# Kernel optimization log

Measured on AMD Instinct MI355X. Metric: run time of the kernel, lower is better.

Reference implementation:

```python
import jax, jax.numpy as jnp
import numpy as np

N = 100000
E = 2000000
F = 64          # in_features == out_features (required by attention * h_j)
BETA = 0.5
NEG_SLOPE = 0.01  # torch F.leaky_relu default


def setup_inputs() -> dict:
    key = jax.random.key(0)
    k1, k2, k3, k4, k5, k6 = jax.random.split(key, 6)
    h = jax.random.normal(k1, (N, F), dtype=jnp.float32)
    adj = jax.random.randint(k2, (2, E), 0, N, dtype=jnp.int64)
    amount = jax.random.uniform(k3, (E,), dtype=jnp.float32)
    count = jax.random.uniform(k4, (E,), dtype=jnp.float32)
    fc_w = jax.random.normal(k5, (F, 2 * F), dtype=jnp.float32) * (1.0 / np.sqrt(2 * F))
    fc_b = jax.random.normal(k6, (F,), dtype=jnp.float32) * 0.01
    return {"h": h, "adj": adj, "amount": amount, "count": count,
            "fc_w": fc_w, "fc_b": fc_b}


def _minmax_norm(x):
    lo, hi = x.min(), x.max()
    return (x - lo) / (hi - lo + 1e-8)


def reference(h, adj, amount, count, fc_w, fc_b):
    # per-edge weight from normalized amount/count
    edge_weight = BETA * _minmax_norm(amount) + (1.0 - BETA) * _minmax_norm(count)  # [E]

    src, dst = adj[0], adj[1]
    h_i = h[src]                     # [E, F]
    h_j = h[dst]                     # [E, F]
    h_cat = jnp.concatenate([h_i, h_j], axis=1)  # [E, 2F]

    score = jnp.einsum('ef,of->eo', h_cat, fc_w) + fc_b  # [E, F_out]
    score = jnp.where(score >= 0, score, NEG_SLOPE * score)  # leaky_relu
    score = score * edge_weight[:, None]

    # softmax over ALL edges (dim 0), per feature, as in the original
    attention = jax.nn.softmax(score, axis=0)  # [E, F]

    agg = jnp.zeros_like(h).at[src].add(attention * h_j)  # scatter-add -> [N, F]
    return agg
```

## Files before the change

kernel.cpp:

```cpp
#include <hip/hip_runtime.h>
#include <hip/hip_fp16.h>
#include <math.h>

#define FDIM   64
#define NB     16
#define BSHIFT 7
#define BMASK  127
#define EPTA   16
#define CHUNKA (EPTA * 256)
#define SCH    1024
#define DMASK  0xFFFFF

__global__ __launch_bounds__(256) void count_mm_k(const int* __restrict__ src,
                                                  const float* __restrict__ amount,
                                                  const float* __restrict__ count,
                                                  int* __restrict__ mat,
                                                  float4* __restrict__ partial,
                                                  double* __restrict__ colsum,
                                                  int E, int nblkA, int nbkt) {
  __shared__ int lhist[1024];
  __shared__ float4 lred[4];
  for (int k = threadIdx.x; k < nbkt; k += 256) lhist[k] = 0;
  if (blockIdx.x == 0 && threadIdx.x < 64) colsum[threadIdx.x] = 0.0;
  __syncthreads();
  float amin = 3.4e38f, amax = -3.4e38f, cmin = 3.4e38f, cmax = -3.4e38f;
  int e0 = blockIdx.x * CHUNKA + threadIdx.x * EPTA;
  if (e0 + EPTA <= E) {
    #pragma unroll
    for (int q = 0; q < EPTA; q += 4) {
      int4   s4 = *(const int4*)(src + e0 + q);
      float4 a4 = *(const float4*)(amount + e0 + q);
      float4 c4 = *(const float4*)(count + e0 + q);
      atomicAdd(&lhist[s4.x >> BSHIFT], 1);
      atomicAdd(&lhist[s4.y >> BSHIFT], 1);
      atomicAdd(&lhist[s4.z >> BSHIFT], 1);
      atomicAdd(&lhist[s4.w >> BSHIFT], 1);
      amin = fminf(amin, fminf(fminf(a4.x, a4.y), fminf(a4.z, a4.w)));
      amax = fmaxf(amax, fmaxf(fmaxf(a4.x, a4.y), fmaxf(a4.z, a4.w)));
      cmin = fminf(cmin, fminf(fminf(c4.x, c4.y), fminf(c4.z, c4.w)));
      cmax = fmaxf(cmax, fmaxf(fmaxf(c4.x, c4.y), fmaxf(c4.z, c4.w)));
    }
  } else {
    for (int e = e0; e < E; e++) {
      atomicAdd(&lhist[src[e] >> BSHIFT], 1);
      float a = amount[e], c = count[e];
      amin = fminf(amin, a); amax = fmaxf(amax, a);
      cmin = fminf(cmin, c); cmax = fmaxf(cmax, c);
    }
  }
  #pragma unroll
  for (int off = 32; off; off >>= 1) {
    amin = fminf(amin, __shfl_down(amin, off));
    amax = fmaxf(amax, __shfl_down(amax, off));
    cmin = fminf(cmin, __shfl_down(cmin, off));
    cmax = fmaxf(cmax, __shfl_down(cmax, off));
  }
  if ((threadIdx.x & 63) == 0) lred[threadIdx.x >> 6] = make_float4(amin, amax, cmin, cmax);
  __syncthreads();
  for (int k = threadIdx.x; k < nbkt; k += 256)
    mat[(size_t)k * nblkA + blockIdx.x] = lhist[k];
  if (threadIdx.x == 0) {
    float4 r = lred[0];
    #pragma unroll
    for (int w = 1; w < 4; w++) {
      r.x = fminf(r.x, lred[w].x); r.y = fmaxf(r.y, lred[w].y);
      r.z = fminf(r.z, lred[w].z); r.w = fmaxf(r.w, lred[w].w);
    }
    partial[blockIdx.x] = r;
  }
}

__global__ __launch_bounds__(256) void minmax2_k(const float4* __restrict__ partial,
                                                 float* __restrict__ mmf, int nb) {
  float amin = 3.4e38f, amax = -3.4e38f, cmin = 3.4e38f, cmax = -3.4e38f;
  for (int i = threadIdx.x; i < nb; i += 256) {
    float4 p = partial[i];
    amin = fminf(amin, p.x); amax = fmaxf(amax, p.y);
    cmin = fminf(cmin, p.z); cmax = fmaxf(cmax, p.w);
  }
  #pragma unroll
  for (int off = 32; off; off >>= 1) {
    amin = fminf(amin, __shfl_down(amin, off));
    amax = fmaxf(amax, __shfl_down(amax, off));
    cmin = fminf(cmin, __shfl_down(cmin, off));
    cmax = fmaxf(cmax, __shfl_down(cmax, off));
  }
  __shared__ float4 lds[4];
  if ((threadIdx.x & 63) == 0) lds[threadIdx.x >> 6] = make_float4(amin, amax, cmin, cmax);
  __syncthreads();
  if (threadIdx.x == 0) {
    float4 r = lds[0];
    #pragma unroll
    for (int w = 1; w < 4; w++) {
      r.x = fminf(r.x, lds[w].x); r.y = fmaxf(r.y, lds[w].y);
      r.z = fminf(r.z, lds[w].z); r.w = fmaxf(r.w, lds[w].w);
    }
    mmf[0] = r.x; mmf[1] = r.y; mmf[2] = r.z; mmf[3] = r.w;
  }
}

__global__ __launch_bounds__(256) void scan1_k(const int* __restrict__ v,
                                               int* __restrict__ bsum, int M) {
  __shared__ int lds[256];
  int t = threadIdx.x, b = blockIdx.x;
  int s = 0;
  for (int i = b * SCH + t; i < min((b + 1) * SCH, M); i += 256) s += v[i];
  lds[t] = s; __syncthreads();
  for (int off = 128; off; off >>= 1) {
    if (t < off) lds[t] += lds[t + off];
    __syncthreads();
  }
  if (t == 0) bsum[b] = lds[0];
}

__global__ __launch_bounds__(256) void scan2_k(const int* __restrict__ bsum,
                                               int* __restrict__ bexcl, int nchunk) {
  __shared__ int lds[256];
  int t = threadIdx.x;
  int running = 0;
  for (int c0 = 0; c0 < nchunk; c0 += 256) {
    int x = (c0 + t < nchunk) ? bsum[c0 + t] : 0;
    lds[t] = x; __syncthreads();
    for (int off = 1; off < 256; off <<= 1) {
      int v = (t >= off) ? lds[t - off] : 0;
      __syncthreads();
      lds[t] += v; __syncthreads();
    }
    if (c0 + t < nchunk) bexcl[c0 + t] = running + lds[t] - x;
    running += lds[255];
    __syncthreads();
  }
}

__global__ __launch_bounds__(256) void scan3_k(const int* __restrict__ v,
                                               const int* __restrict__ bexcl,
                                               int* __restrict__ smat, int M) {
  __shared__ int lds[256];
  int t = threadIdx.x, b = blockIdx.x;
  int running = bexcl[b];
  for (int tile = 0; tile < SCH; tile += 256) {
    int i = b * SCH + tile + t;
    int x = (i < M) ? v[i] : 0;
    lds[t] = x; __syncthreads();
    for (int off = 1; off < 256; off <<= 1) {
      int vv = (t >= off) ? lds[t - off] : 0;
      __syncthreads();
      lds[t] += vv; __syncthreads();
    }
    if (i < M) smat[i] = running + lds[t] - x;
    running += lds[255];
    __syncthreads();
  }
}

__global__ __launch_bounds__(256) void scatter_k(const int* __restrict__ src,
                                                 const int* __restrict__ dst,
                                                 const float* __restrict__ amount,
                                                 const float* __restrict__ count,
                                                 const float* __restrict__ mmf,
                                                 const int* __restrict__ smat,
                                                 int2* __restrict__ payload,
                                                 int E, int nblkA, int nbkt) {
  __shared__ int cntb[1024];
  __shared__ int baseb[1024];
  __shared__ int sbase[1024];
  __shared__ int tmp[256];
  __shared__ int2 lpay[CHUNKA];
  __shared__ int lgpos[CHUNKA];
  const int t = threadIdx.x, blk = blockIdx.x;
  for (int k = t; k < nbkt; k += 256) {
    cntb[k] = 0;
    sbase[k] = smat[(size_t)k * nblkA + blk];
  }
  __syncthreads();
  const float amin = mmf[0], amax = mmf[1], cmin = mmf[2], cmax = mmf[3];
  const float ascale = 0.5f / (amax - amin + 1e-8f);
  const float cscale = 0.5f / (cmax - cmin + 1e-8f);
  int e0 = blk * CHUNKA + t * EPTA;
  const bool full = (e0 + EPTA <= E);
  int4   S[4]; int4 D[4]; float4 A[4]; float4 C[4];
  if (full) {
    #pragma unroll
    for (int q = 0; q < 4; q++) {
      S[q] = *(const int4*)(src + e0 + 4 * q);
      D[q] = *(const int4*)(dst + e0 + 4 * q);
      A[q] = *(const float4*)(amount + e0 + 4 * q);
      C[q] = *(const float4*)(count + e0 + 4 * q);
      atomicAdd(&cntb[S[q].x >> BSHIFT], 1);
      atomicAdd(&cntb[S[q].y >> BSHIFT], 1);
      atomicAdd(&cntb[S[q].z >> BSHIFT], 1);
      atomicAdd(&cntb[S[q].w >> BSHIFT], 1);
    }
  } else {
    for (int e = e0; e < E; e++) atomicAdd(&cntb[src[e] >> BSHIFT], 1);
  }
  __syncthreads();
  int running = 0;
  for (int c0 = 0; c0 < nbkt; c0 += 256) {
    int x = (c0 + t < nbkt) ? cntb[c0 + t] : 0;
    tmp[t] = x; __syncthreads();
    for (int off = 1; off < 256; off <<= 1) {
      int v = (t >= off) ? tmp[t - off] : 0;
      __syncthreads();
      tmp[t] += v; __syncthreads();
    }
    if (c0 + t < nbkt) baseb[c0 + t] = running + tmp[t] - x;
    running += tmp[255];
    __syncthreads();
  }
  for (int k = t; k < nbkt; k += 256) cntb[k] = baseb[k];
  __syncthreads();
  auto ins = [&](int s, int d, float a, float c) {
    int b = s >> BSHIFT;
    float ew = (a - amin) * ascale + (c - cmin) * cscale;
    int pos = atomicAdd(&cntb[b], 1);
    lpay[pos] = make_int2(d | ((s & BMASK) << 20), __float_as_int(ew));
    lgpos[pos] = sbase[b] + (pos - baseb[b]);
  };
  if (full) {
    #pragma unroll
    for (int q = 0; q < 4; q++) {
      ins(S[q].x, D[q].x, A[q].x, C[q].x);
      ins(S[q].y, D[q].y, A[q].y, C[q].y);
      ins(S[q].z, D[q].z, A[q].z, C[q].z);
      ins(S[q].w, D[q].w, A[q].w, C[q].w);
    }
  } else {
    for (int e = e0; e < E; e++) ins(src[e], dst[e], amount[e], count[e]);
  }
  __syncthreads();
  const int ned = min(CHUNKA, E - blk * CHUNKA);
  for (int i = t; i < ned; i += 256) payload[lgpos[i]] = lpay[i];
}

__global__ __launch_bounds__(256) void binB_k(const int2* __restrict__ payload,
                                              const int* __restrict__ smat,
                                              int* __restrict__ hist,
                                              int* __restrict__ offsets,
                                              int2* __restrict__ edge_s,
                                              int E, int nblkA, int nbkt, int N) {
  __shared__ int fcnt[128];
  __shared__ int fs[128];
  __shared__ int fcur[128];
  const int b = blockIdx.x;
  const int t = threadIdx.x;
  const int base = smat[(size_t)b * nblkA];
  const int end  = (b + 1 < nbkt) ? smat[(size_t)(b + 1) * nblkA] : E;
  if (t < 128) fcnt[t] = 0;
  __syncthreads();
  for (int i = base + t; i < end; i += 256)
    atomicAdd(&fcnt[payload[i].x >> 20], 1);
  __syncthreads();
  if (t < 128) fs[t] = fcnt[t];
  __syncthreads();
  for (int off = 1; off < 128; off <<= 1) {
    int v = 0;
    if (t < 128 && t >= off) v = fs[t - off];
    __syncthreads();
    if (t < 128) fs[t] += v;
    __syncthreads();
  }
  if (t < 128) {
    int excl = fs[t] - fcnt[t];
    fcur[t] = base + excl;
    int node = (b << BSHIFT) + t;
    if (node < N) { hist[node] = fcnt[t]; offsets[node] = base + excl; }
  }
  __syncthreads();
  for (int i = base + t; i < end; i += 256) {
    int2 v = payload[i];
    int pos = atomicAdd(&fcur[v.x >> 20], 1);
    edge_s[pos] = make_int2(v.x & DMASK, v.y);
  }
}

__global__ __launch_bounds__(128) void pre_gemm(const float* __restrict__ h,
                                                const float* __restrict__ fc_w,
                                                const float* __restrict__ fc_b,
                                                float* __restrict__ G1,
                                                __half2* __restrict__ P, int N) {
  __shared__ float hs[NB * FDIM];
  const int t = threadIdx.x;
  const int o = t & 63, half = t >> 6;
  float w[FDIM];
  const float* wrow = fc_w + o * 128 + half * 64;
  #pragma unroll
  for (int f = 0; f < FDIM; f += 4) {
    float4 v = *(const float4*)(wrow + f);
    w[f] = v.x; w[f + 1] = v.y; w[f + 2] = v.z; w[f + 3] = v.w;
  }
  const float bias = (half == 0) ? fc_b[o] : 0.0f;
  const int n0 = blockIdx.x * NB;
  const int nrows = min(NB, N - n0);
  for (int i = t; i < nrows * FDIM; i += 128) hs[i] = h[(size_t)n0 * FDIM + i];
  __syncthreads();
  for (int n = 0; n < nrows; n++) {
    float acc = bias;
    #pragma unroll
    for (int f = 0; f < FDIM; f += 4) {
      float4 hv = *(const float4*)(&hs[n * FDIM + f]);
      acc += hv.x * w[f] + hv.y * w[f + 1] + hv.z * w[f + 2] + hv.w * w[f + 3];
    }
    if (half == 0) {
      G1[(size_t)(n0 + n) * FDIM + o] = acc;
    } else {
      P[(size_t)(n0 + n) * FDIM + o] =
          __halves2half2(__float2half(acc), __float2half(hs[n * FDIM + o]));
    }
  }
}

__device__ __forceinline__ float2 unpack_h2(unsigned u) {
  __half2 v = *(__half2*)&u;
  return make_float2(__low2float(v), __high2float(v));
}

__global__ __launch_bounds__(256) void fused_k(const int* __restrict__ offsets,
                                               const int* __restrict__ hist,
                                               const int2* __restrict__ edge_s,
                                               const float* __restrict__ G1,
                                               const unsigned* __restrict__ P,
                                               double* __restrict__ colsum,
                                               float* __restrict__ out, int N) {
  const int lane = threadIdx.x & 63;
  const int wid = blockIdx.x * 4 + (threadIdx.x >> 6);
  const int nw = gridDim.x * 4;
  float csum = 0.0f;
  int n = wid;
  int start = 0, cnt = 0;
  int2 p0 = make_int2(0, 0);
  float g1 = 0.0f;
  if (n < N) {
    start = offsets[n]; cnt = hist[n];
    g1 = G1[(size_t)n * FDIM + lane];
    if (lane < cnt) p0 = edge_s[start + lane];
  }
  while (n < N) {
    int nn = n + nw;
    int startN = 0, cntN = 0; float g1N = 0.0f;
    if (nn < N) {
      startN = offsets[nn]; cntN = hist[nn];
      g1N = G1[(size_t)nn * FDIM + lane];
    }
    float acc = 0.0f;
    for (int j0 = 0; j0 < cnt; j0 += 64) {
      int m = min(64, cnt - j0);
      int2 p;
      if (j0 == 0) p = p0;
      else { p = make_int2(0, 0); if (lane < m) p = edge_s[start + j0 + lane]; }
      for (int j = 0; j < m; j += 8) {
        int rem = m - j;
        int dd[8]; float ee[8], wm[8]; unsigned uu[8];
        #pragma unroll
        for (int k = 0; k < 8; k++) {
          dd[k] = __builtin_amdgcn_readlane(p.x, j + k);
          ee[k] = __int_as_float(__builtin_amdgcn_readlane(p.y, j + k));
          wm[k] = (k < rem) ? 1.0f : 0.0f;
        }
        #pragma unroll
        for (int k = 0; k < 8; k++) uu[k] = P[(size_t)dd[k] * FDIM + lane];
        #pragma unroll
        for (int k = 0; k < 8; k++) {
          float2 v = unpack_h2(uu[k]);
          float sc = g1 + v.x;
          sc = (sc >= 0.0f) ? sc : 0.01f * sc;
          float x = __expf(sc * ee[k]) * wm[k];
          csum += x;
          acc += x * v.y;
        }
      }
    }
    out[(size_t)n * FDIM + lane] = acc;
    n = nn; start = startN; cnt = cntN; g1 = g1N;
    p0 = make_int2(0, 0);
    if (n < N && lane < min(cnt, 64)) p0 = edge_s[start + lane];
  }
  __shared__ float part[256];
  part[threadIdx.x] = csum;
  __syncthreads();
  if (threadIdx.x < 64) {
    float tot = part[threadIdx.x] + part[threadIdx.x + 64] +
                part[threadIdx.x + 128] + part[threadIdx.x + 192];
    atomicAdd(&colsum[threadIdx.x], (double)tot);
  }
}

__global__ __launch_bounds__(256) void scale_k(float4* __restrict__ out4,
                                               const double* __restrict__ colsum,
                                               int total4) {
  __shared__ float rinv_s[64];
  if (threadIdx.x < 64) rinv_s[threadIdx.x] = (float)(1.0 / colsum[threadIdx.x]);
  __syncthreads();
  const float4* r4 = (const float4*)rinv_s;
  int idx = blockIdx.x * blockDim.x + threadIdx.x;
  int stride = gridDim.x * blockDim.x;
  for (int i = idx; i < total4; i += stride) {
    float4 v = out4[i];
    float4 r = r4[i & 15];
    v.x *= r.x; v.y *= r.y; v.z *= r.z; v.w *= r.w;
    out4[i] = v;
  }
}

extern "C" void kernel_launch(void* const* d_in, const int* in_sizes, int n_in,
                              void* d_out, int out_size, void* d_ws, size_t ws_size,
                              hipStream_t stream) {
  const float* h      = (const float*)d_in[0];
  const int*   adj    = (const int*)d_in[1];
  const float* amount = (const float*)d_in[2];
  const float* count  = (const float*)d_in[3];
  const float* fc_w   = (const float*)d_in[4];
  const float* fc_b   = (const float*)d_in[5];
  float* out = (float*)d_out;

  const int E = in_sizes[2];
  const int N = in_sizes[0] / FDIM;
  const int* src = adj;
  const int* dst = adj + E;
  const int nbkt  = (N + BMASK) >> BSHIFT;
  const int nblkA = (E + CHUNKA - 1) / CHUNKA;
  const int M = nbkt * nblkA;
  const int nchunk = (M + SCH - 1) / SCH;

  char* ws = (char*)d_ws;
  size_t off = 0;
  auto alloc = [&](size_t bytes) { void* p = ws + off; off += (bytes + 255) & ~(size_t)255; return p; };
  float*    G1      = (float*)alloc((size_t)N * FDIM * sizeof(float));
  __half2*  P       = (__half2*)alloc((size_t)N * FDIM * sizeof(__half2));
  int2*     edge_s  = (int2*)alloc((size_t)E * sizeof(int2));
  int2*     payload = (int2*)alloc((size_t)E * sizeof(int2));
  int*      hist    = (int*)alloc((size_t)N * sizeof(int));
  int*      offsets = (int*)alloc((size_t)N * sizeof(int));
  int*      mat     = (int*)alloc((size_t)M * sizeof(int));
  int*      smat    = (int*)alloc((size_t)M * sizeof(int));
  int*      bsum    = (int*)alloc((size_t)nchunk * sizeof(int));
  int*      bexcl   = (int*)alloc((size_t)nchunk * sizeof(int));
  float4*   mmpart  = (float4*)alloc((size_t)nblkA * sizeof(float4));
  double*   colsum  = (double*)alloc(64 * sizeof(double));
  float*    mmf     = (float*)alloc(4 * sizeof(float));

  count_mm_k<<<nblkA, 256, 0, stream>>>(src, amount, count, mat, mmpart, colsum, E, nblkA, nbkt);
  minmax2_k<<<1, 256, 0, stream>>>(mmpart, mmf, nblkA);
  scan1_k<<<nchunk, 256, 0, stream>>>(mat, bsum, M);
  scan2_k<<<1, 256, 0, stream>>>(bsum, bexcl, nchunk);
  scan3_k<<<nchunk, 256, 0, stream>>>(mat, bexcl, smat, M);
  scatter_k<<<nblkA, 256, 0, stream>>>(src, dst, amount, count, mmf, smat, payload, E, nblkA, nbkt);
  binB_k<<<nbkt, 256, 0, stream>>>(payload, smat, hist, offsets, edge_s, E, nblkA, nbkt, N);
  pre_gemm<<<(N + NB - 1) / NB, 128, 0, stream>>>(h, fc_w, fc_b, G1, P, N);
  fused_k<<<4096, 256, 0, stream>>>(offsets, hist, edge_s, G1, (const unsigned*)P, colsum, out, N);
  scale_k<<<1024, 256, 0, stream>>>((float4*)out, colsum, N * FDIM / 4);
}
```

Before: 325.6 us.

## Merge minmax into scan2, unroll gather by 16, pad colsum atomics

The single-block min/max reduction is folded into the single-block scan2 kernel, which saves one launch. The fused aggregation loop no longer prefetches the next node's metadata. It gains a 16-wide unrolled gather path for full groups, and exp is computed with exp2 by folding log2(e) into the edge scale. The per-column double atomics are spread to a stride of 16 doubles so they land on separate cache lines. Dropping the cross-node prefetch may expose latency that the deeper unroll is meant to hide.

Measured after the change: 306.8 us. 5.8% less time.

```diff
diff --git a/kernel.cpp b/kernel.cpp
--- a/kernel.cpp
+++ b/kernel.cpp
@@ -21,7 +21,8 @@
   __shared__ int lhist[1024];
   __shared__ float4 lred[4];
   for (int k = threadIdx.x; k < nbkt; k += 256) lhist[k] = 0;
-  if (blockIdx.x == 0 && threadIdx.x < 64) colsum[threadIdx.x] = 0.0;
+  if (blockIdx.x == 0)
+    for (int i = threadIdx.x; i < 1024; i += 256) colsum[i] = 0.0;
   __syncthreads();
   float amin = 3.4e38f, amax = -3.4e38f, cmin = 3.4e38f, cmax = -3.4e38f;
   int e0 = blockIdx.x * CHUNKA + threadIdx.x * EPTA;
@@ -70,35 +71,6 @@
   }
 }
 
-__global__ __launch_bounds__(256) void minmax2_k(const float4* __restrict__ partial,
-                                                 float* __restrict__ mmf, int nb) {
-  float amin = 3.4e38f, amax = -3.4e38f, cmin = 3.4e38f, cmax = -3.4e38f;
-  for (int i = threadIdx.x; i < nb; i += 256) {
-    float4 p = partial[i];
-    amin = fminf(amin, p.x); amax = fmaxf(amax, p.y);
-    cmin = fminf(cmin, p.z); cmax = fmaxf(cmax, p.w);
-  }
-  #pragma unroll
-  for (int off = 32; off; off >>= 1) {
-    amin = fminf(amin, __shfl_down(amin, off));
-    amax = fmaxf(amax, __shfl_down(amax, off));
-    cmin = fminf(cmin, __shfl_down(cmin, off));
-    cmax = fmaxf(cmax, __shfl_down(cmax, off));
-  }
-  __shared__ float4 lds[4];
-  if ((threadIdx.x & 63) == 0) lds[threadIdx.x >> 6] = make_float4(amin, amax, cmin, cmax);
-  __syncthreads();
-  if (threadIdx.x == 0) {
-    float4 r = lds[0];
-    #pragma unroll
-    for (int w = 1; w < 4; w++) {
-      r.x = fminf(r.x, lds[w].x); r.y = fmaxf(r.y, lds[w].y);
-      r.z = fminf(r.z, lds[w].z); r.w = fmaxf(r.w, lds[w].w);
-    }
-    mmf[0] = r.x; mmf[1] = r.y; mmf[2] = r.z; mmf[3] = r.w;
-  }
-}
-
 __global__ __launch_bounds__(256) void scan1_k(const int* __restrict__ v,
                                                int* __restrict__ bsum, int M) {
   __shared__ int lds[256];
@@ -114,7 +86,9 @@
 }
 
 __global__ __launch_bounds__(256) void scan2_k(const int* __restrict__ bsum,
-                                               int* __restrict__ bexcl, int nchunk) {
+                                               int* __restrict__ bexcl, int nchunk,
+                                               const float4* __restrict__ partial,
+                                               float* __restrict__ mmf, int nb) {
   __shared__ int lds[256];
   int t = threadIdx.x;
   int running = 0;
@@ -129,6 +103,31 @@
     if (c0 + t < nchunk) bexcl[c0 + t] = running + lds[t] - x;
     running += lds[255];
     __syncthreads();
+  }
+  float amin = 3.4e38f, amax = -3.4e38f, cmin = 3.4e38f, cmax = -3.4e38f;
+  for (int i = t; i < nb; i += 256) {
+    float4 p = partial[i];
+    amin = fminf(amin, p.x); amax = fmaxf(amax, p.y);
+    cmin = fminf(cmin, p.z); cmax = fmaxf(cmax, p.w);
+  }
+  #pragma unroll
+  for (int off = 32; off; off >>= 1) {
+    amin = fminf(amin, __shfl_down(amin, off));
+    amax = fmaxf(amax, __shfl_down(amax, off));
+    cmin = fminf(cmin, __shfl_down(cmin, off));
+    cmax = fmaxf(cmax, __shfl_down(cmax, off));
+  }
+  __shared__ float4 lred[4];
+  if ((t & 63) == 0) lred[t >> 6] = make_float4(amin, amax, cmin, cmax);
+  __syncthreads();
+  if (t == 0) {
+    float4 r = lred[0];
+    #pragma unroll
+    for (int w = 1; w < 4; w++) {
+      r.x = fminf(r.x, lred[w].x); r.y = fmaxf(r.y, lred[w].y);
+      r.z = fminf(r.z, lred[w].z); r.w = fmaxf(r.w, lred[w].w);
+    }
+    mmf[0] = r.x; mmf[1] = r.y; mmf[2] = r.z; mmf[3] = r.w;
   }
 }
 
@@ -174,11 +173,12 @@
   }
   __syncthreads();
   const float amin = mmf[0], amax = mmf[1], cmin = mmf[2], cmax = mmf[3];
-  const float ascale = 0.5f / (amax - amin + 1e-8f);
-  const float cscale = 0.5f / (cmax - cmin + 1e-8f);
+  const float L2E = 1.4426950408889634f;
+  const float ascale = 0.5f * L2E / (amax - amin + 1e-8f);
+  const float cscale = 0.5f * L2E / (cmax - cmin + 1e-8f);
   int e0 = blk * CHUNKA + t * EPTA;
   const bool full = (e0 + EPTA <= E);
-  int4   S[4]; int4 D[4]; float4 A[4]; float4 C[4];
+  int4 S[4]; int4 D[4]; float4 A[4]; float4 C[4];
   if (full) {
     #pragma unroll
     for (int q = 0; q < 4; q++) {
@@ -326,29 +326,35 @@
   const int wid = blockIdx.x * 4 + (threadIdx.x >> 6);
   const int nw = gridDim.x * 4;
   float csum = 0.0f;
-  int n = wid;
-  int start = 0, cnt = 0;
-  int2 p0 = make_int2(0, 0);
-  float g1 = 0.0f;
-  if (n < N) {
-    start = offsets[n]; cnt = hist[n];
-    g1 = G1[(size_t)n * FDIM + lane];
-    if (lane < cnt) p0 = edge_s[start + lane];
-  }
-  while (n < N) {
-    int nn = n + nw;
-    int startN = 0, cntN = 0; float g1N = 0.0f;
-    if (nn < N) {
-      startN = offsets[nn]; cntN = hist[nn];
-      g1N = G1[(size_t)nn * FDIM + lane];
-    }
+  for (int n = wid; n < N; n += nw) {
+    float g1 = G1[(size_t)n * FDIM + lane];
     float acc = 0.0f;
+    int start = offsets[n], cnt = hist[n];
     for (int j0 = 0; j0 < cnt; j0 += 64) {
       int m = min(64, cnt - j0);
-      int2 p;
-      if (j0 == 0) p = p0;
-      else { p = make_int2(0, 0); if (lane < m) p = edge_s[start + j0 + lane]; }
-      for (int j = 0; j < m; j += 8) {
+      int2 p = make_int2(0, 0);
+      if (lane < m) p = edge_s[start + j0 + lane];
+      int j = 0;
+      for (; j + 16 <= m; j += 16) {
+        int dd[16]; float ee[16]; unsigned uu[16];
+        #pragma unroll
+        for (int k = 0; k < 16; k++) {
+          dd[k] = __builtin_amdgcn_readlane(p.x, j + k);
+          ee[k] = __int_as_float(__builtin_amdgcn_readlane(p.y, j + k));
+        }
+        #pragma unroll
+        for (int k = 0; k < 16; k++) uu[k] = P[(size_t)dd[k] * FDIM + lane];
+        #pragma unroll
+        for (int k = 0; k < 16; k++) {
+          float2 v = unpack_h2(uu[k]);
+          float sc = g1 + v.x;
+          sc = fmaxf(sc, 0.01f * sc);
+          float x = exp2f(sc * ee[k]);
+          csum += x;
+          acc += x * v.y;
+        }
+      }
+      for (; j < m; j += 8) {
         int rem = m - j;
         int dd[8]; float ee[8], wm[8]; unsigned uu[8];
         #pragma unroll
@@ -363,17 +369,14 @@
         for (int k = 0; k < 8; k++) {
           float2 v = unpack_h2(uu[k]);
           float sc = g1 + v.x;
-          sc = (sc >= 0.0f) ? sc : 0.01f * sc;
-          float x = __expf(sc * ee[k]) * wm[k];
+          sc = fmaxf(sc, 0.01f * sc);
+          float x = exp2f(sc * ee[k]) * wm[k];
           csum += x;
           acc += x * v.y;
         }
       }
     }
     out[(size_t)n * FDIM + lane] = acc;
-    n = nn; start = startN; cnt = cntN; g1 = g1N;
-    p0 = make_int2(0, 0);
-    if (n < N && lane < min(cnt, 64)) p0 = edge_s[start + lane];
   }
   __shared__ float part[256];
   part[threadIdx.x] = csum;
@@ -381,7 +384,7 @@
   if (threadIdx.x < 64) {
     float tot = part[threadIdx.x] + part[threadIdx.x + 64] +
                 part[threadIdx.x + 128] + part[threadIdx.x + 192];
-    atomicAdd(&colsum[threadIdx.x], (double)tot);
+    atomicAdd(&colsum[threadIdx.x * 16], (double)tot);
   }
 }
 
@@ -389,7 +392,7 @@
                                                const double* __restrict__ colsum,
                                                int total4) {
   __shared__ float rinv_s[64];
-  if (threadIdx.x < 64) rinv_s[threadIdx.x] = (float)(1.0 / colsum[threadIdx.x]);
+  if (threadIdx.x < 64) rinv_s[threadIdx.x] = (float)(1.0 / colsum[threadIdx.x * 16]);
   __syncthreads();
   const float4* r4 = (const float4*)rinv_s;
   int idx = blockIdx.x * blockDim.x + threadIdx.x;
@@ -436,13 +439,12 @@
   int*      bsum    = (int*)alloc((size_t)nchunk * sizeof(int));
   int*      bexcl   = (int*)alloc((size_t)nchunk * sizeof(int));
   float4*   mmpart  = (float4*)alloc((size_t)nblkA * sizeof(float4));
-  double*   colsum  = (double*)alloc(64 * sizeof(double));
+  double*   colsum  = (double*)alloc(1024 * sizeof(double));
   float*    mmf     = (float*)alloc(4 * sizeof(float));
 
   count_mm_k<<<nblkA, 256, 0, stream>>>(src, amount, count, mat, mmpart, colsum, E, nblkA, nbkt);
-  minmax2_k<<<1, 256, 0, stream>>>(mmpart, mmf, nblkA);
   scan1_k<<<nchunk, 256, 0, stream>>>(mat, bsum, M);
-  scan2_k<<<1, 256, 0, stream>>>(bsum, bexcl, nchunk);
+  scan2_k<<<1, 256, 0, stream>>>(bsum, bexcl, nchunk, mmpart, mmf, nblkA);
   scan3_k<<<nchunk, 256, 0, stream>>>(mat, bexcl, smat, M);
   scatter_k<<<nblkA, 256, 0, stream>>>(src, dst, amount, count, mmf, smat, payload, E, nblkA, nbkt);
   binB_k<<<nbkt, 256, 0, stream>>>(payload, smat, hist, offsets, edge_s, E, nblkA, nbkt, N);
```
